# Optimization experiments

Hardware: AMD Instinct MI355X
Metric: run time of the kernel (lower is better)

Reference implementation:

```python
import jax, jax.numpy as jnp
import numpy as np

N_NODES = 100000
N_EDGES = 3200000
D_IN = 128
D_OUT = 128

def setup_inputs() -> dict:
    key = jax.random.key(0)
    k1, k2, k3, k4, k5 = jax.random.split(key, 5)
    nodes = jnp.arange(N_NODES, dtype=jnp.int64 if jax.config.jax_enable_x64 else jnp.int32)
    features = jax.random.normal(k1, (N_NODES, D_IN), dtype=jnp.float32)
    edge_index = jax.random.randint(k2, (2, N_EDGES), 0, N_NODES)
    # torch nn.Linear(2*D_IN, D_OUT) params, stored as [in, out]
    bound = 1.0 / np.sqrt(2 * D_IN)
    W = jax.random.uniform(k3, (2 * D_IN, D_OUT), minval=-bound, maxval=bound, dtype=jnp.float32)
    b = jax.random.uniform(k4, (D_OUT,), minval=-bound, maxval=bound, dtype=jnp.float32)
    return {"nodes": nodes, "features": features, "edge_index": edge_index, "W": W, "b": b}

def reference(nodes, features, edge_index, W, b):
    # Mean aggregation over full neighbor lists. gcn=False: edges are treated
    # as undirected (neighbors appended for both src and dst), and output is
    # relu(Linear(concat([self_feats, neigh_feats]))).
    N, d = features.shape
    src, dst = edge_index[0], edge_index[1]
    neigh_sum = (jnp.zeros((N, d), features.dtype)
                 .at[src].add(features[dst])
                 .at[dst].add(features[src]))
    cnt = (jnp.zeros((N,), features.dtype)
           .at[src].add(1.0)
           .at[dst].add(1.0))
    neigh_mean = neigh_sum / jnp.maximum(cnt, 1.0)[:, None]
    combined = jnp.concatenate([features[nodes], neigh_mean[nodes]], axis=1)  # [B, 2d]
    return jax.nn.relu(combined @ W + b)
```

## Files before the change

### kernel.cpp

```cpp
#include <hip/hip_runtime.h>
#include <hip/hip_bf16.h>
#include <cmath>

#define D 128
#define MAXNB 1024
#define TEDGE 4096
#define BSH 8
#define BNODES 256
#define CURPAD 16

typedef __attribute__((ext_vector_type(8))) short bf16x8;
typedef __attribute__((ext_vector_type(4))) float f32x4;
typedef __attribute__((ext_vector_type(2))) float f32x2;

__device__ __forceinline__ unsigned short f2bf(float f) {
    union { __hip_bfloat16 h; unsigned short u; } c;
    c.h = __float2bfloat16(f);
    return c.u;
}

__device__ __forceinline__ void accum8(float* a, uint4 u) {
    a[0] += __uint_as_float(u.x << 16);
    a[1] += __uint_as_float(u.x & 0xffff0000u);
    a[2] += __uint_as_float(u.y << 16);
    a[3] += __uint_as_float(u.y & 0xffff0000u);
    a[4] += __uint_as_float(u.z << 16);
    a[5] += __uint_as_float(u.z & 0xffff0000u);
    a[6] += __uint_as_float(u.w << 16);
    a[7] += __uint_as_float(u.w & 0xffff0000u);
}

__device__ __forceinline__ void accum8f8v(f32x2* a, uint2 u) {
    a[0] += __builtin_amdgcn_cvt_pk_f32_fp8((int)u.x, false);
    a[1] += __builtin_amdgcn_cvt_pk_f32_fp8((int)u.x, true);
    a[2] += __builtin_amdgcn_cvt_pk_f32_fp8((int)u.y, false);
    a[3] += __builtin_amdgcn_cvt_pk_f32_fp8((int)u.y, true);
}

__global__ __launch_bounds__(256) void partition_edges(
    const int* __restrict__ ei, int* __restrict__ cursor,
    int* __restrict__ arena, int pbcap, int E, int nb) {
    __shared__ int cnt[MAXNB];
    __shared__ int off[MAXNB + 1];
    __shared__ int gb[MAXNB];
    __shared__ int sb[256];
    __shared__ int stage[2 * TEDGE];
    const int t = threadIdx.x;
    const int e0 = blockIdx.x * TEDGE;
    const int eE = min(e0 + TEDGE, E);

#pragma unroll
    for (int k = 0; k < 4; ++k) cnt[t * 4 + k] = 0;
    __syncthreads();

    int s[16], d[16];
    bool v[16];
#pragma unroll
    for (int q = 0; q < 16; ++q) {
        int e = e0 + t + q * 256;
        v[q] = e < eE;
        if (v[q]) { s[q] = ei[e]; d[q] = ei[E + e]; }
    }

#pragma unroll
    for (int q = 0; q < 16; ++q) if (v[q]) {
        atomicAdd(&cnt[s[q] >> BSH], 1);
        atomicAdd(&cnt[d[q] >> BSH], 1);
    }
    __syncthreads();

    int c0 = cnt[t * 4], c1 = cnt[t * 4 + 1], c2 = cnt[t * 4 + 2], c3 = cnt[t * 4 + 3];
    sb[t] = c0 + c1 + c2 + c3;
    __syncthreads();
    for (int o = 1; o < 256; o <<= 1) {
        int x = (t >= o) ? sb[t - o] : 0;
        __syncthreads();
        sb[t] += x;
        __syncthreads();
    }
    int run = (t > 0) ? sb[t - 1] : 0;
    off[t * 4] = run; run += c0;
    off[t * 4 + 1] = run; run += c1;
    off[t * 4 + 2] = run; run += c2;
    off[t * 4 + 3] = run;
    if (t == 255) off[MAXNB] = sb[255];

    for (int j = t; j < nb; j += 256) {
        int c = cnt[j];
        gb[j] = c ? atomicAdd(&cursor[j * CURPAD], c) : 0;
    }
    __syncthreads();

#pragma unroll
    for (int k = 0; k < 4; ++k) cnt[t * 4 + k] = off[t * 4 + k];
    __syncthreads();

#pragma unroll
    for (int q = 0; q < 16; ++q) if (v[q]) {
        int ps = atomicAdd(&cnt[s[q] >> BSH], 1);
        stage[ps] = ((s[q] & (BNODES - 1)) << 17) | d[q];
        int pd = atomicAdd(&cnt[d[q] >> BSH], 1);
        stage[pd] = ((d[q] & (BNODES - 1)) << 17) | s[q];
    }
    __syncthreads();

    const int total = 2 * (eE - e0);
    for (int p = t; p < total; p += 256) {
        int vv = stage[p];
        int lo = 0, hi = MAXNB;
        while (hi - lo > 1) {
            int mid = (lo + hi) >> 1;
            if (off[mid] <= p) lo = mid; else hi = mid;
        }
        int idx = gb[lo] + (p - off[lo]);
        if (idx < pbcap) arena[(size_t)lo * pbcap + idx] = vv;
    }
}

__global__ __launch_bounds__(512) void bucket_scatter(
    const int* __restrict__ cursor, const int* __restrict__ arena, int pbcap,
    int* __restrict__ deg, int* __restrict__ colp, int cap, int N, int nb) {
    __shared__ int ldeg[BNODES];
    const int t = threadIdx.x;
    for (int b = blockIdx.x; b < nb; b += gridDim.x) {
        if (t < BNODES) ldeg[t] = 0;
        __syncthreads();
        int cnt = cursor[b * CURPAD];
        if (cnt > pbcap) cnt = pbcap;
        const int* s = arena + (size_t)b * pbcap;
        const size_t cb = ((size_t)b << BSH) * cap;
        int i = t;
        for (; i + 1536 < cnt; i += 2048) {
            int v0 = s[i], v1 = s[i + 512], v2 = s[i + 1024], v3 = s[i + 1536];
            int r0 = atomicAdd(&ldeg[v0 >> 17], 1);
            int r1 = atomicAdd(&ldeg[v1 >> 17], 1);
            int r2 = atomicAdd(&ldeg[v2 >> 17], 1);
            int r3 = atomicAdd(&ldeg[v3 >> 17], 1);
            if (r0 < cap) colp[cb + (size_t)(v0 >> 17) * cap + r0] = v0 & 0x1FFFF;
            if (r1 < cap) colp[cb + (size_t)(v1 >> 17) * cap + r1] = v1 & 0x1FFFF;
            if (r2 < cap) colp[cb + (size_t)(v2 >> 17) * cap + r2] = v2 & 0x1FFFF;
            if (r3 < cap) colp[cb + (size_t)(v3 >> 17) * cap + r3] = v3 & 0x1FFFF;
        }
        for (; i < cnt; i += 512) {
            int v = s[i];
            int r = atomicAdd(&ldeg[v >> 17], 1);
            if (r < cap) colp[cb + (size_t)(v >> 17) * cap + r] = v & 0x1FFFF;
        }
        __syncthreads();
        if (t < BNODES) {
            int node = (b << BSH) + t;
            if (node < N) deg[node] = ldeg[t];
        }
        __syncthreads();
    }
}

__global__ __launch_bounds__(256) void bucket_fill(
    const int* __restrict__ ei, int* __restrict__ deg,
    int* __restrict__ colp, int cap, int E) {
    int tid = blockIdx.x * blockDim.x + threadIdx.x;
    int stride = gridDim.x * blockDim.x;
    int e[8], s[8], d[8];
    bool v[8];
#pragma unroll
    for (int q = 0; q < 8; ++q) {
        e[q] = tid + q * stride;
        v[q] = e[q] < E;
    }
#pragma unroll
    for (int q = 0; q < 8; ++q) if (v[q]) { s[q] = ei[e[q]]; d[q] = ei[E + e[q]]; }
    int rs[8], rd[8];
#pragma unroll
    for (int q = 0; q < 8; ++q) if (v[q]) rs[q] = atomicAdd(&deg[s[q]], 1);
#pragma unroll
    for (int q = 0; q < 8; ++q) if (v[q]) rd[q] = atomicAdd(&deg[d[q]], 1);
#pragma unroll
    for (int q = 0; q < 8; ++q) if (v[q] && rs[q] < cap) colp[(size_t)s[q] * cap + rs[q]] = d[q];
#pragma unroll
    for (int q = 0; q < 8; ++q) if (v[q] && rd[q] < cap) colp[(size_t)d[q] * cap + rd[q]] = s[q];
}

__global__ __launch_bounds__(256) void prep_all(
    const float* __restrict__ feat, const float* __restrict__ W,
    int* __restrict__ cursor, uint2* __restrict__ f8,
    unsigned* __restrict__ wb, int n8) {
    const int tid = blockIdx.x * blockDim.x + threadIdx.x;
    const int stride = gridDim.x * blockDim.x;

    for (int i = tid; i < 1024 * CURPAD; i += stride) cursor[i] = 0;

    for (int id = tid; id < 4096; id += stride) {
        int j = id & 127, ks = id >> 7;
        unsigned hi[4], lo[4];
#pragma unroll
        for (int e = 0; e < 4; ++e) {
            float w0 = W[(size_t)(ks * 8 + 2 * e) * 128 + j];
            float w1 = W[(size_t)(ks * 8 + 2 * e + 1) * 128 + j];
            unsigned short h0 = f2bf(w0), h1 = f2bf(w1);
            float l0f = w0 - __uint_as_float((unsigned)h0 << 16);
            float l1f = w1 - __uint_as_float((unsigned)h1 << 16);
            hi[e] = (unsigned)h0 | ((unsigned)h1 << 16);
            lo[e] = (unsigned)f2bf(l0f) | ((unsigned)f2bf(l1f) << 16);
        }
        ((uint4*)wb)[ks * 128 + j] = make_uint4(hi[0], hi[1], hi[2], hi[3]);
        ((uint4*)wb)[4096 + ks * 128 + j] = make_uint4(lo[0], lo[1], lo[2], lo[3]);
    }

    const float4* f = (const float4*)feat;
    for (int i = tid; i < n8; i += stride) {
        float4 a = f[2 * i];
        float4 c = f[2 * i + 1];
        int w0 = __builtin_amdgcn_cvt_pk_fp8_f32(a.x, a.y, 0, false);
        w0 = __builtin_amdgcn_cvt_pk_fp8_f32(a.z, a.w, w0, true);
        int w1 = __builtin_amdgcn_cvt_pk_fp8_f32(c.x, c.y, 0, false);
        w1 = __builtin_amdgcn_cvt_pk_fp8_f32(c.z, c.w, w1, true);
        uint2 r;
        r.x = (unsigned)w0;
        r.y = (unsigned)w1;
        f8[i] = r;
    }
}

__global__ __launch_bounds__(256) void convert_fp8(
    const float4* __restrict__ f, uint2* __restrict__ o, int n8) {
    int i = blockIdx.x * blockDim.x + threadIdx.x;
    int stride = gridDim.x * blockDim.x;
    for (; i < n8; i += stride) {
        float4 a = f[2 * i];
        float4 c = f[2 * i + 1];
        int w0 = __builtin_amdgcn_cvt_pk_fp8_f32(a.x, a.y, 0, false);
        w0 = __builtin_amdgcn_cvt_pk_fp8_f32(a.z, a.w, w0, true);
        int w1 = __builtin_amdgcn_cvt_pk_fp8_f32(c.x, c.y, 0, false);
        w1 = __builtin_amdgcn_cvt_pk_fp8_f32(c.z, c.w, w1, true);
        uint2 r;
        r.x = (unsigned)w0;
        r.y = (unsigned)w1;
        o[i] = r;
    }
}

__global__ __launch_bounds__(256) void convert_bf16(
    const float4* __restrict__ f, uint2* __restrict__ o, int n4) {
    int i = blockIdx.x * blockDim.x + threadIdx.x;
    int stride = gridDim.x * blockDim.x;
    for (; i < n4; i += stride) {
        float4 v = f[i];
        uint2 r;
        r.x = (unsigned)f2bf(v.x) | ((unsigned)f2bf(v.y) << 16);
        r.y = (unsigned)f2bf(v.z) | ((unsigned)f2bf(v.w) << 16);
        o[i] = r;
    }
}

__global__ __launch_bounds__(256) void prepack_w(
    const float* __restrict__ W, unsigned* __restrict__ wb) {
    int id = blockIdx.x * 256 + threadIdx.x;
    if (id >= 4096) return;
    int j = id & 127, ks = id >> 7;
    unsigned hi[4], lo[4];
#pragma unroll
    for (int e = 0; e < 4; ++e) {
        float w0 = W[(size_t)(ks * 8 + 2 * e) * 128 + j];
        float w1 = W[(size_t)(ks * 8 + 2 * e + 1) * 128 + j];
        unsigned short h0 = f2bf(w0), h1 = f2bf(w1);
        float l0f = w0 - __uint_as_float((unsigned)h0 << 16);
        float l1f = w1 - __uint_as_float((unsigned)h1 << 16);
        hi[e] = (unsigned)h0 | ((unsigned)h1 << 16);
        lo[e] = (unsigned)f2bf(l0f) | ((unsigned)f2bf(l1f) << 16);
    }
    ((uint4*)wb)[ks * 128 + j] = make_uint4(hi[0], hi[1], hi[2], hi[3]);
    ((uint4*)wb)[4096 + ks * 128 + j] = make_uint4(lo[0], lo[1], lo[2], lo[3]);
}

__global__ __launch_bounds__(256) void gather_gemm_pad(
    const int* __restrict__ nodes, const float* __restrict__ feat,
    const uint2* __restrict__ fb2,
    const int* __restrict__ deg, const int* __restrict__ colp, int cap,
    const uint4* __restrict__ wb4, const float* __restrict__ b,
    float* __restrict__ out, int B) {
    __shared__ uint4 combQ[512];
    unsigned char* combB = (unsigned char*)combQ;
    const int t = threadIdx.x;
    const int lane = t & 63;
    const int w = t >> 6;
    const int g = lane >> 4;
    const int sub = lane & 15;
    const int base = blockIdx.x * 16;

    {
        int r = t >> 4, sb = t & 15;
        int row = base + r;
        uint4 u = make_uint4(0u, 0u, 0u, 0u);
        if (row < B) {
            const float* fp = feat + (size_t)nodes[row] * D + sb * 8;
            float4 a = *(const float4*)fp;
            float4 c = *(const float4*)(fp + 4);
            u.x = (unsigned)f2bf(a.x) | ((unsigned)f2bf(a.y) << 16);
            u.y = (unsigned)f2bf(a.z) | ((unsigned)f2bf(a.w) << 16);
            u.z = (unsigned)f2bf(c.x) | ((unsigned)f2bf(c.y) << 16);
            u.w = (unsigned)f2bf(c.z) | ((unsigned)f2bf(c.w) << 16);
        }
        int off = (r * 512 + sb * 16) ^ ((r & 7) << 4);
        *(uint4*)(combB + off) = u;
    }

    for (int rq = 0; rq < 4; ++rq) {
        const int rl = w + 4 * rq;
        const int row = base + rl;
        if (row < B) {
            const int node = __builtin_amdgcn_readfirstlane(nodes[row]);
            int degn = deg[node];
            if (degn > cap) degn = cap;
            const int p0 = node * cap;
            f32x2 accA[4] = {{0.f, 0.f}, {0.f, 0.f}, {0.f, 0.f}, {0.f, 0.f}};
            f32x2 accB[4] = {{0.f, 0.f}, {0.f, 0.f}, {0.f, 0.f}, {0.f, 0.f}};
            int i = 0;
            int nn0 = 0, nn1 = 0, nn2 = 0, nn3 = 0;
            if (degn >= 16) {
                nn0 = colp[p0 + g];
                nn1 = colp[p0 + 4 + g];
                nn2 = colp[p0 + 8 + g];
                nn3 = colp[p0 + 12 + g];
            }
            for (; i + 15 < degn; i += 16) {
                int n0 = nn0, n1 = nn1, n2 = nn2, n3 = nn3;
                if (i + 31 < degn) {
                    nn0 = colp[p0 + i + 16 + g];
                    nn1 = colp[p0 + i + 20 + g];
                    nn2 = colp[p0 + i + 24 + g];
                    nn3 = colp[p0 + i + 28 + g];
                }
                uint2 u0 = fb2[(size_t)n0 * 16 + sub];
                uint2 u1 = fb2[(size_t)n1 * 16 + sub];
                uint2 u2 = fb2[(size_t)n2 * 16 + sub];
                uint2 u3 = fb2[(size_t)n3 * 16 + sub];
                accum8f8v(accA, u0);
                accum8f8v(accB, u1);
                accum8f8v(accA, u2);
                accum8f8v(accB, u3);
            }
            for (; i + 7 < degn; i += 8) {
                int n0 = colp[p0 + i + g];
                int n1 = colp[p0 + i + 4 + g];
                uint2 u0 = fb2[(size_t)n0 * 16 + sub];
                uint2 u1 = fb2[(size_t)n1 * 16 + sub];
                accum8f8v(accA, u0);
                accum8f8v(accB, u1);
            }
            for (; i + 3 < degn; i += 4) {
                int n0 = colp[p0 + i + g];
                accum8f8v(accA, fb2[(size_t)n0 * 16 + sub]);
            }
            int rem = degn - i;
            if (g < rem) {
                int n0 = colp[p0 + i + g];
                accum8f8v(accB, fb2[(size_t)n0 * 16 + sub]);
            }
            const float inv = (degn > 0) ? 1.0f / (float)degn : 0.0f;
            float vals[8];
#pragma unroll
            for (int k = 0; k < 4; ++k) {
                f32x2 v2 = accA[k] + accB[k];
                float vx = v2.x, vy = v2.y;
                vx += __shfl_xor(vx, 16, 64);
                vx += __shfl_xor(vx, 32, 64);
                vy += __shfl_xor(vy, 16, 64);
                vy += __shfl_xor(vy, 32, 64);
                vals[2 * k] = vx * inv;
                vals[2 * k + 1] = vy * inv;
            }
            if (g == 0) {
                unsigned p0u = (unsigned)f2bf(vals[0]) | ((unsigned)f2bf(vals[1]) << 16);
                unsigned p1u = (unsigned)f2bf(vals[2]) | ((unsigned)f2bf(vals[3]) << 16);
                unsigned p2u = (unsigned)f2bf(vals[4]) | ((unsigned)f2bf(vals[5]) << 16);
                unsigned p3u = (unsigned)f2bf(vals[6]) | ((unsigned)f2bf(vals[7]) << 16);
                int off = (rl * 512 + 256 + sub * 16) ^ ((rl & 7) << 4);
                *(uint4*)(combB + off) = make_uint4(p0u, p1u, p2u, p3u);
            }
        } else if (g == 0) {
            int off = (rl * 512 + 256 + sub * 16) ^ ((rl & 7) << 4);
            *(uint4*)(combB + off) = make_uint4(0u, 0u, 0u, 0u);
        }
    }
    __syncthreads();

    const int jl = lane & 15;
    const int kg = lane >> 4;
    const int j0 = w * 32 + jl, j1 = j0 + 16;
    f32x4 acc0 = {0.f, 0.f, 0.f, 0.f};
    f32x4 acc1 = {0.f, 0.f, 0.f, 0.f};
#pragma unroll
    for (int s = 0; s < 8; ++s) {
        int aoff = (jl * 512 + s * 64 + kg * 16) ^ ((jl & 7) << 4);
        bf16x8 a = *(const bf16x8*)(combB + aoff);
        int bi = (s * 4 + kg) * 128;
        bf16x8 bh0 = *(const bf16x8*)&wb4[bi + j0];
        bf16x8 bh1 = *(const bf16x8*)&wb4[bi + j1];
        bf16x8 bl0 = *(const bf16x8*)&wb4[4096 + bi + j0];
        bf16x8 bl1 = *(const bf16x8*)&wb4[4096 + bi + j1];
        acc0 = __builtin_amdgcn_mfma_f32_16x16x32_bf16(a, bh0, acc0, 0, 0, 0);
        acc1 = __builtin_amdgcn_mfma_f32_16x16x32_bf16(a, bh1, acc1, 0, 0, 0);
        acc0 = __builtin_amdgcn_mfma_f32_16x16x32_bf16(a, bl0, acc0, 0, 0, 0);
        acc1 = __builtin_amdgcn_mfma_f32_16x16x32_bf16(a, bl1, acc1, 0, 0, 0);
    }
    const float b0 = b[j0], b1 = b[j1];
    const int r0 = kg * 4;
#pragma unroll
    for (int rg = 0; rg < 4; ++rg) {
        int row = base + r0 + rg;
        if (row < B) {
            out[(size_t)row * D + j0] = fmaxf(acc0[rg] + b0, 0.0f);
            out[(size_t)row * D + j1] = fmaxf(acc1[rg] + b1, 0.0f);
        }
    }
}


__global__ __launch_bounds__(256) void deg_rank(
    const int* __restrict__ ei, int* __restrict__ deg,
    unsigned* __restrict__ rank, int E) {
    int tid = blockIdx.x * blockDim.x + threadIdx.x;
    int stride = gridDim.x * blockDim.x;
    int e[8], s[8], d[8];
    bool v[8];
#pragma unroll
    for (int q = 0; q < 8; ++q) {
        e[q] = tid + q * stride;
        v[q] = e[q] < E;
    }
#pragma unroll
    for (int q = 0; q < 8; ++q) if (v[q]) { s[q] = ei[e[q]]; d[q] = ei[E + e[q]]; }
    int rs[8], rd[8];
#pragma unroll
    for (int q = 0; q < 8; ++q) if (v[q]) rs[q] = atomicAdd(&deg[s[q]], 1);
#pragma unroll
    for (int q = 0; q < 8; ++q) if (v[q]) rd[q] = atomicAdd(&deg[d[q]], 1);
#pragma unroll
    for (int q = 0; q < 8; ++q)
        if (v[q]) rank[e[q]] = (unsigned)rs[q] | ((unsigned)rd[q] << 16);
}

__global__ __launch_bounds__(256) void scan_block(
    const int* __restrict__ deg, int* __restrict__ rowptr,
    int* __restrict__ bsum, int N) {
    __shared__ int lds[256];
    const int t = threadIdx.x;
    const int base = blockIdx.x * 1024 + t * 4;
    int v[4];
#pragma unroll
    for (int k = 0; k < 4; ++k) v[k] = (base + k < N) ? deg[base + k] : 0;
    lds[t] = v[0] + v[1] + v[2] + v[3];
    __syncthreads();
    for (int off = 1; off < 256; off <<= 1) {
        int x = (t >= off) ? lds[t - off] : 0;
        __syncthreads();
        lds[t] += x;
        __syncthreads();
    }
    if (t == 255) bsum[blockIdx.x] = lds[255];
    int run = (t > 0) ? lds[t - 1] : 0;
#pragma unroll
    for (int k = 0; k < 4; ++k) {
        if (base + k < N) rowptr[base + k] = run;
        run += v[k];
    }
}

__global__ __launch_bounds__(1024) void scan_aux(int* __restrict__ bsum, int nb) {
    __shared__ int lds[1024];
    const int t = threadIdx.x;
    int v = (t < nb) ? bsum[t] : 0;
    lds[t] = v;
    __syncthreads();
    for (int off = 1; off < 1024; off <<= 1) {
        int x = (t >= off) ? lds[t - off] : 0;
        __syncthreads();
        lds[t] += x;
        __syncthreads();
    }
    if (t < nb) bsum[t] = lds[t] - v;
}

__global__ __launch_bounds__(256) void scan_finalize(
    int* __restrict__ rowptr, const int* __restrict__ bsum, int N, int twoE) {
    int i = blockIdx.x * blockDim.x + threadIdx.x;
    if (i == 0) rowptr[N] = twoE;
    if (i >= N) return;
    rowptr[i] += bsum[i >> 10];
}

__global__ __launch_bounds__(256) void csr_fill2(
    const int* __restrict__ ei, const int* __restrict__ rowptr,
    const unsigned* __restrict__ rank, int* __restrict__ col, int E) {
    int tid = blockIdx.x * blockDim.x + threadIdx.x;
    int stride = gridDim.x * blockDim.x;
    int e[8], s[8], d[8], ps[8], pd[8];
    unsigned r[8];
    bool v[8];
#pragma unroll
    for (int q = 0; q < 8; ++q) {
        e[q] = tid + q * stride;
        v[q] = e[q] < E;
    }
#pragma unroll
    for (int q = 0; q < 8; ++q) if (v[q]) { s[q] = ei[e[q]]; d[q] = ei[E + e[q]]; r[q] = rank[e[q]]; }
#pragma unroll
    for (int q = 0; q < 8; ++q) if (v[q]) { ps[q] = rowptr[s[q]]; pd[q] = rowptr[d[q]]; }
#pragma unroll
    for (int q = 0; q < 8; ++q) if (v[q]) {
        col[ps[q] + (int)(r[q] & 0xffffu)] = d[q];
        col[pd[q] + (int)(r[q] >> 16)] = s[q];
    }
}

__global__ __launch_bounds__(256) void gather_gemm(
    const int* __restrict__ nodes, const uint4* __restrict__ fb4,
    const int* __restrict__ rowptr, const int* __restrict__ col,
    const float* __restrict__ W, const float* __restrict__ b,
    float* __restrict__ out, int B) {
    __shared__ float comb[16][256];
    const int t = threadIdx.x;
    const int lane = t & 63;
    const int w = t >> 6;
    const int g = lane >> 4;
    const int sub = lane & 15;
    const int base = blockIdx.x * 16;
    {
        int r = t >> 4, sb = t & 15;
        int row = base + r;
        float a[8] = {0, 0, 0, 0, 0, 0, 0, 0};
        if (row < B) accum8(a, fb4[(size_t)nodes[row] * 16 + sb]);
        *(float4*)&comb[r][sb * 8] = make_float4(a[0], a[1], a[2], a[3]);
        *(float4*)&comb[r][sb * 8 + 4] = make_float4(a[4], a[5], a[6], a[7]);
    }
    for (int rq = 0; rq < 4; ++rq) {
        const int rl = w + 4 * rq;
        const int row = base + rl;
        if (row < B) {
            const int node = __builtin_amdgcn_readfirstlane(nodes[row]);
            const int p0 = rowptr[node], p1 = rowptr[node + 1];
            float accA[8] = {0, 0, 0, 0, 0, 0, 0, 0};
            float accB[8] = {0, 0, 0, 0, 0, 0, 0, 0};
            int i = p0;
            for (; i + 7 < p1; i += 8) {
                int na = col[i + g];
                int nb = col[i + 4 + g];
                uint4 ua = fb4[(size_t)na * 16 + sub];
                uint4 ub = fb4[(size_t)nb * 16 + sub];
                accum8(accA, ua);
                accum8(accB, ub);
            }
            for (; i + 3 < p1; i += 4) {
                int na = col[i + g];
                accum8(accA, fb4[(size_t)na * 16 + sub]);
            }
            int rem = p1 - i;
            if (g < rem) {
                int na = col[i + g];
                accum8(accB, fb4[(size_t)na * 16 + sub]);
            }
            const int degn = p1 - p0;
            const float inv = (degn > 0) ? 1.0f / (float)degn : 0.0f;
            float vals[8];
#pragma unroll
            for (int k = 0; k < 8; ++k) {
                float v = accA[k] + accB[k];
                v += __shfl_xor(v, 16, 64);
                v += __shfl_xor(v, 32, 64);
                vals[k] = v * inv;
            }
            if (g == 0) {
                *(float4*)&comb[rl][128 + sub * 8] =
                    make_float4(vals[0], vals[1], vals[2], vals[3]);
                *(float4*)&comb[rl][128 + sub * 8 + 4] =
                    make_float4(vals[4], vals[5], vals[6], vals[7]);
            }
        } else if (g == 0) {
            float4 z = make_float4(0.f, 0.f, 0.f, 0.f);
            *(float4*)&comb[rl][128 + sub * 8] = z;
            *(float4*)&comb[rl][128 + sub * 8 + 4] = z;
        }
    }
    __syncthreads();
    const int j = t & 127;
    const int rr = t >> 7;
    float acc[8];
    const float bj = b[j];
#pragma unroll
    for (int r = 0; r < 8; ++r) acc[r] = bj;
    for (int k4 = 0; k4 < 64; ++k4) {
        float w0 = W[(size_t)(4 * k4 + 0) * 128 + j];
        float w1 = W[(size_t)(4 * k4 + 1) * 128 + j];
        float w2 = W[(size_t)(4 * k4 + 2) * 128 + j];
        float w3 = W[(size_t)(4 * k4 + 3) * 128 + j];
#pragma unroll
        for (int r = 0; r < 8; ++r) {
            float4 c = *(const float4*)&comb[2 * r + rr][4 * k4];
            acc[r] = fmaf(c.x, w0, acc[r]);
            acc[r] = fmaf(c.y, w1, acc[r]);
            acc[r] = fmaf(c.z, w2, acc[r]);
            acc[r] = fmaf(c.w, w3, acc[r]);
        }
    }
#pragma unroll
    for (int r = 0; r < 8; ++r) {
        int row = base + 2 * r + rr;
        if (row < B) out[(size_t)row * D + j] = fmaxf(acc[r], 0.0f);
    }
}

__global__ __launch_bounds__(256) void edge_scatter(
    const int* __restrict__ ei, const float* __restrict__ feat,
    float* __restrict__ nsum, float* __restrict__ cnt, int E) {
    long long tid = (long long)blockIdx.x * blockDim.x + threadIdx.x;
    int e = (int)(tid >> 7);
    if (e >= E) return;
    int d = (int)(tid & 127);
    int src = ei[e];
    int dst = ei[E + e];
    atomicAdd(&nsum[(size_t)src * D + d], feat[(size_t)dst * D + d]);
    atomicAdd(&nsum[(size_t)dst * D + d], feat[(size_t)src * D + d]);
    if (d == 0) {
        atomicAdd(&cnt[src], 1.0f);
        atomicAdd(&cnt[dst], 1.0f);
    }
}

__global__ __launch_bounds__(256) void sage_out(
    const int* __restrict__ nodes, const float* __restrict__ feat,
    const float* nsum, const float* __restrict__ cnt,
    const float* __restrict__ W, const float* __restrict__ b,
    float* out, int B) {
    __shared__ float comb[16][256];
    const int t = threadIdx.x;
    const int j = t & 127;
    const int rr = t >> 7;
    const int base = blockIdx.x * 16;
    for (int r = 0; r < 16; ++r) {
        int row = base + r;
        float v = 0.0f;
        if (row < B) {
            int node = nodes[row];
            if (t < 128) v = feat[(size_t)node * D + t];
            else v = nsum[(size_t)node * D + (t - 128)] / fmaxf(cnt[node], 1.0f);
        }
        comb[r][t] = v;
    }
    __syncthreads();
    float acc[8];
    const float bj = b[j];
#pragma unroll
    for (int r = 0; r < 8; ++r) acc[r] = bj;
#pragma unroll 4
    for (int k = 0; k < 256; ++k) {
        float wj = W[(size_t)k * 128 + j];
#pragma unroll
        for (int r = 0; r < 8; ++r) acc[r] += comb[rr + 2 * r][k] * wj;
    }
#pragma unroll
    for (int r = 0; r < 8; ++r) {
        int row = base + rr + 2 * r;
        if (row < B) out[(size_t)row * D + j] = fmaxf(acc[r], 0.0f);
    }
}

extern "C" void kernel_launch(void* const* d_in, const int* in_sizes, int n_in,
                              void* d_out, int out_size, void* d_ws, size_t ws_size,
                              hipStream_t stream) {
    const int* nodes = (const int*)d_in[0];
    const float* feat = (const float*)d_in[1];
    const int* ei = (const int*)d_in[2];
    const float* W = (const float*)d_in[3];
    const float* b = (const float*)d_in[4];
    float* out = (float*)d_out;

    const int B = in_sizes[0];
    const int N = in_sizes[1] / D;
    const int E = in_sizes[2] / 2;
    const int twoE = 2 * E;
    const int nscan = (N + 1023) / 1024;
    const int n4 = N * (D / 4);
    const int n8 = N * (D / 8);
    const size_t ws_ints = ws_size / sizeof(int);

    const int nb = (N + BNODES - 1) >> BSH;
    double avgpb = nb > 0 ? (2.0 * (double)E) / (double)nb : 0.0;
    int pbcap = (int)(avgpb + 8.0 * sqrt(avgpb > 0.0 ? avgpb : 0.0) + 64.0);
    pbcap = (pbcap + 3) & ~3;
    const size_t u_arena = (size_t)nb * pbcap;
    const size_t u_fp8 = (size_t)N * 32;
    const size_t u0 = (u_arena > u_fp8) ? u_arena : u_fp8;
    const size_t o0_deg = (u0 + 3) & ~(size_t)3;
    const size_t o0_cur = (o0_deg + N + 3) & ~(size_t)3;
    const size_t o0_wb = o0_cur + 1024 * CURPAD;
    const size_t o0_colp = o0_wb + 32768;
    long long cap0_ll = (ws_ints > o0_colp) ? (long long)((ws_ints - o0_colp) / N) : 0;
    int cap0 = (cap0_ll > 192) ? 192 : (int)cap0_ll;

    const size_t o1_deg = (size_t)N * 32;
    const size_t o1_wb = (o1_deg + N + 3) & ~(size_t)3;
    const size_t o1_colp = o1_wb + 32768;
    long long cap_ll = (ws_ints > o1_colp) ? (long long)((ws_ints - o1_colp) / N) : 0;
    int cap = (cap_ll > 192) ? 192 : (int)cap_ll;

    const size_t o_deg = 0;
    const size_t o_rowptr = (o_deg + N + 3) & ~(size_t)3;
    const size_t o_bsum = (o_rowptr + N + 1 + 3) & ~(size_t)3;
    const size_t o_col = (o_bsum + 1024 + 3) & ~(size_t)3;
    const size_t o_rank = (o_col + twoE + 3) & ~(size_t)3;
    const size_t tail = ((size_t)E > (size_t)N * 64) ? (size_t)E : (size_t)N * 64;
    const size_t need2 = (o_rank + tail) * sizeof(int);

    if (cap0 >= 128 && N <= (1 << 17) && nb <= MAXNB && E > 0) {
        int* wsI = (int*)d_ws;
        int* arena = wsI;
        unsigned* f8 = (unsigned*)wsI;
        int* deg = wsI + o0_deg;
        int* cursor = wsI + o0_cur;
        unsigned* wbp = (unsigned*)(wsI + o0_wb);
        int* colp = wsI + o0_colp;

        prep_all<<<64, 256, 0, stream>>>(feat, W, cursor, (uint2*)f8, wbp, 0);

        int pblocks = (E + TEDGE - 1) / TEDGE;
        partition_edges<<<pblocks, 256, 0, stream>>>(ei, cursor, arena, pbcap, E, nb);

        bucket_scatter<<<nb, 512, 0, stream>>>(
            cursor, arena, pbcap, deg, colp, cap0, N, nb);

        convert_fp8<<<(n8 + 1023) / 1024, 256, 0, stream>>>(
            (const float4*)feat, (uint2*)f8, n8);

        gather_gemm_pad<<<(B + 15) / 16, 256, 0, stream>>>(
            nodes, feat, (const uint2*)f8, deg, colp, cap0,
            (const uint4*)wbp, b, out, B);
    } else if (cap >= 128) {
        int* wsI = (int*)d_ws;
        unsigned* f8 = (unsigned*)wsI;
        int* deg = wsI + o1_deg;
        unsigned* wbp = (unsigned*)(wsI + o1_wb);
        int* colp = wsI + o1_colp;

        hipMemsetAsync(deg, 0, (size_t)N * sizeof(int), stream);

        prepack_w<<<16, 256, 0, stream>>>(W, wbp);

        convert_fp8<<<(n8 + 1023) / 1024, 256, 0, stream>>>(
            (const float4*)feat, (uint2*)f8, n8);

        int eb8 = (E + 2047) / 2048;
        bucket_fill<<<eb8, 256, 0, stream>>>(ei, deg, colp, cap, E);

        gather_gemm_pad<<<(B + 15) / 16, 256, 0, stream>>>(
            nodes, feat, (const uint2*)f8, deg, colp, cap,
            (const uint4*)wbp, b, out, B);
    } else if (ws_size >= need2 && nscan <= 1024) {
        int* wsI = (int*)d_ws;
        int* deg = wsI + o_deg;
        int* rowptr = wsI + o_rowptr;
        int* bsum = wsI + o_bsum;
        int* col = wsI + o_col;
        unsigned* rank = (unsigned*)(wsI + o_rank);
        unsigned* fbu = (unsigned*)(wsI + o_rank);

        hipMemsetAsync(deg, 0, (size_t)N * sizeof(int), stream);

        int eb8 = (E + 2047) / 2048;
        deg_rank<<<eb8, 256, 0, stream>>>(ei, deg, rank, E);
        scan_block<<<nscan, 256, 0, stream>>>(deg, rowptr, bsum, N);
        scan_aux<<<1, 1024, 0, stream>>>(bsum, nscan);
        scan_finalize<<<(N + 255) / 256, 256, 0, stream>>>(rowptr, bsum, N, twoE);
        csr_fill2<<<eb8, 256, 0, stream>>>(ei, rowptr, rank, col, E);
        convert_bf16<<<(n4 + 1023) / 1024, 256, 0, stream>>>(
            (const float4*)feat, (uint2*)fbu, n4);
        gather_gemm<<<(B + 15) / 16, 256, 0, stream>>>(
            nodes, (const uint4*)fbu, rowptr, col, W, b, out, B);
    } else {
        float* nsum = out;
        float* cnt = (float*)d_ws;
        hipMemsetAsync(d_out, 0, (size_t)N * D * sizeof(float), stream);
        hipMemsetAsync(d_ws, 0, (size_t)N * sizeof(float), stream);
        long long tot = (long long)E * 128;
        int blocks = (int)((tot + 255) / 256);
        edge_scatter<<<blocks, 256, 0, stream>>>(ei, feat, nsum, cnt, E);
        sage_out<<<(B + 15) / 16, 256, 0, stream>>>(nodes, feat, nsum, cnt, W, b, out, B);
    }
}
```

Measured before the change: 381.1 us.

## Fuse fp8 conversion into bucket_scatter and stage neighbor lists in LDS

Gives the fp8 feature buffer its own workspace region so it no longer aliases the edge arena. That lets extra blocks of the bucket_scatter launch run the fp32-to-fp8 conversion alongside the scatter, which removes the separate convert_fp8 launch. The gather kernel now preloads per-row degrees and column indices into LDS with coalesced loads before the gather loop, in place of the per-wave register prefetch from global memory. This costs more workspace, which gates the new path, and more LDS per block, which may reduce occupancy.

```diff
diff --git a/kernel.cpp b/kernel.cpp
--- a/kernel.cpp
+++ b/kernel.cpp
@@ -8,6 +8,7 @@
 #define BSH 8
 #define BNODES 256
 #define CURPAD 16
+#define LCS 200
 
 typedef __attribute__((ext_vector_type(8))) short bf16x8;
 typedef __attribute__((ext_vector_type(4))) float f32x4;
@@ -119,39 +120,56 @@
 
 __global__ __launch_bounds__(512) void bucket_scatter(
     const int* __restrict__ cursor, const int* __restrict__ arena, int pbcap,
-    int* __restrict__ deg, int* __restrict__ colp, int cap, int N, int nb) {
+    int* __restrict__ deg, int* __restrict__ colp, int cap, int N, int nb,
+    const float4* __restrict__ feat4, uint2* __restrict__ f8, int n8, int nconv) {
     __shared__ int ldeg[BNODES];
     const int t = threadIdx.x;
-    for (int b = blockIdx.x; b < nb; b += gridDim.x) {
-        if (t < BNODES) ldeg[t] = 0;
-        __syncthreads();
-        int cnt = cursor[b * CURPAD];
-        if (cnt > pbcap) cnt = pbcap;
-        const int* s = arena + (size_t)b * pbcap;
-        const size_t cb = ((size_t)b << BSH) * cap;
-        int i = t;
-        for (; i + 1536 < cnt; i += 2048) {
-            int v0 = s[i], v1 = s[i + 512], v2 = s[i + 1024], v3 = s[i + 1536];
-            int r0 = atomicAdd(&ldeg[v0 >> 17], 1);
-            int r1 = atomicAdd(&ldeg[v1 >> 17], 1);
-            int r2 = atomicAdd(&ldeg[v2 >> 17], 1);
-            int r3 = atomicAdd(&ldeg[v3 >> 17], 1);
-            if (r0 < cap) colp[cb + (size_t)(v0 >> 17) * cap + r0] = v0 & 0x1FFFF;
-            if (r1 < cap) colp[cb + (size_t)(v1 >> 17) * cap + r1] = v1 & 0x1FFFF;
-            if (r2 < cap) colp[cb + (size_t)(v2 >> 17) * cap + r2] = v2 & 0x1FFFF;
-            if (r3 < cap) colp[cb + (size_t)(v3 >> 17) * cap + r3] = v3 & 0x1FFFF;
-        }
-        for (; i < cnt; i += 512) {
-            int v = s[i];
-            int r = atomicAdd(&ldeg[v >> 17], 1);
-            if (r < cap) colp[cb + (size_t)(v >> 17) * cap + r] = v & 0x1FFFF;
-        }
-        __syncthreads();
-        if (t < BNODES) {
-            int node = (b << BSH) + t;
-            if (node < N) deg[node] = ldeg[t];
-        }
-        __syncthreads();
+    const int bx = (int)blockIdx.x;
+    if (bx >= nb) {
+        int i = (bx - nb) * (int)blockDim.x + t;
+        const int stride = nconv * (int)blockDim.x;
+        for (; i < n8; i += stride) {
+            float4 a = feat4[2 * i];
+            float4 c = feat4[2 * i + 1];
+            int w0 = __builtin_amdgcn_cvt_pk_fp8_f32(a.x, a.y, 0, false);
+            w0 = __builtin_amdgcn_cvt_pk_fp8_f32(a.z, a.w, w0, true);
+            int w1 = __builtin_amdgcn_cvt_pk_fp8_f32(c.x, c.y, 0, false);
+            w1 = __builtin_amdgcn_cvt_pk_fp8_f32(c.z, c.w, w1, true);
+            uint2 r;
+            r.x = (unsigned)w0;
+            r.y = (unsigned)w1;
+            f8[i] = r;
+        }
+        return;
+    }
+    const int b = bx;
+    if (t < BNODES) ldeg[t] = 0;
+    __syncthreads();
+    int cnt = cursor[b * CURPAD];
+    if (cnt > pbcap) cnt = pbcap;
+    const int* s = arena + (size_t)b * pbcap;
+    const size_t cb = ((size_t)b << BSH) * cap;
+    int i = t;
+    for (; i + 1536 < cnt; i += 2048) {
+        int v0 = s[i], v1 = s[i + 512], v2 = s[i + 1024], v3 = s[i + 1536];
+        int r0 = atomicAdd(&ldeg[v0 >> 17], 1);
+        int r1 = atomicAdd(&ldeg[v1 >> 17], 1);
+        int r2 = atomicAdd(&ldeg[v2 >> 17], 1);
+        int r3 = atomicAdd(&ldeg[v3 >> 17], 1);
+        if (r0 < cap) colp[cb + (size_t)(v0 >> 17) * cap + r0] = v0 & 0x1FFFF;
+        if (r1 < cap) colp[cb + (size_t)(v1 >> 17) * cap + r1] = v1 & 0x1FFFF;
+        if (r2 < cap) colp[cb + (size_t)(v2 >> 17) * cap + r2] = v2 & 0x1FFFF;
+        if (r3 < cap) colp[cb + (size_t)(v3 >> 17) * cap + r3] = v3 & 0x1FFFF;
+    }
+    for (; i < cnt; i += 512) {
+        int v = s[i];
+        int r = atomicAdd(&ldeg[v >> 17], 1);
+        if (r < cap) colp[cb + (size_t)(v >> 17) * cap + r] = v & 0x1FFFF;
+    }
+    __syncthreads();
+    if (t < BNODES) {
+        int node = (b << BSH) + t;
+        if (node < N) deg[node] = ldeg[t];
     }
 }
 
@@ -279,6 +297,8 @@
     const uint4* __restrict__ wb4, const float* __restrict__ b,
     float* __restrict__ out, int B) {
     __shared__ uint4 combQ[512];
+    __shared__ int sdeg[16];
+    __shared__ int lcol[16 * LCS];
     unsigned char* combB = (unsigned char*)combQ;
     const int t = threadIdx.x;
     const int lane = t & 63;
@@ -287,6 +307,15 @@
     const int sub = lane & 15;
     const int base = blockIdx.x * 16;
 
+    if (t < 16) {
+        int row = base + t;
+        int dgv = 0;
+        if (row < B) {
+            dgv = deg[nodes[row]];
+            if (dgv > cap) dgv = cap;
+        }
+        sdeg[t] = dgv;
+    }
     {
         int r = t >> 4, sb = t & 15;
         int row = base + r;
@@ -303,83 +332,77 @@
         int off = (r * 512 + sb * 16) ^ ((r & 7) << 4);
         *(uint4*)(combB + off) = u;
     }
+    __syncthreads();
+
+    {
+        int r = t >> 4, l = t & 15;
+        int row = base + r;
+        int dgv = sdeg[r];
+        if (row < B && dgv > 0) {
+            int p0 = nodes[row] * cap;
+            for (int i = l; i < dgv; i += 16) lcol[r * LCS + i] = colp[p0 + i];
+        }
+    }
+    __syncthreads();
 
     for (int rq = 0; rq < 4; ++rq) {
         const int rl = w + 4 * rq;
-        const int row = base + rl;
-        if (row < B) {
-            const int node = __builtin_amdgcn_readfirstlane(nodes[row]);
-            int degn = deg[node];
-            if (degn > cap) degn = cap;
-            const int p0 = node * cap;
-            f32x2 accA[4] = {{0.f, 0.f}, {0.f, 0.f}, {0.f, 0.f}, {0.f, 0.f}};
-            f32x2 accB[4] = {{0.f, 0.f}, {0.f, 0.f}, {0.f, 0.f}, {0.f, 0.f}};
-            int i = 0;
-            int nn0 = 0, nn1 = 0, nn2 = 0, nn3 = 0;
-            if (degn >= 16) {
-                nn0 = colp[p0 + g];
-                nn1 = colp[p0 + 4 + g];
-                nn2 = colp[p0 + 8 + g];
-                nn3 = colp[p0 + 12 + g];
-            }
-            for (; i + 15 < degn; i += 16) {
-                int n0 = nn0, n1 = nn1, n2 = nn2, n3 = nn3;
-                if (i + 31 < degn) {
-                    nn0 = colp[p0 + i + 16 + g];
-                    nn1 = colp[p0 + i + 20 + g];
-                    nn2 = colp[p0 + i + 24 + g];
-                    nn3 = colp[p0 + i + 28 + g];
-                }
-                uint2 u0 = fb2[(size_t)n0 * 16 + sub];
-                uint2 u1 = fb2[(size_t)n1 * 16 + sub];
-                uint2 u2 = fb2[(size_t)n2 * 16 + sub];
-                uint2 u3 = fb2[(size_t)n3 * 16 + sub];
-                accum8f8v(accA, u0);
-                accum8f8v(accB, u1);
-                accum8f8v(accA, u2);
-                accum8f8v(accB, u3);
-            }
-            for (; i + 7 < degn; i += 8) {
-                int n0 = colp[p0 + i + g];
-                int n1 = colp[p0 + i + 4 + g];
-                uint2 u0 = fb2[(size_t)n0 * 16 + sub];
-                uint2 u1 = fb2[(size_t)n1 * 16 + sub];
-                accum8f8v(accA, u0);
-                accum8f8v(accB, u1);
-            }
-            for (; i + 3 < degn; i += 4) {
-                int n0 = colp[p0 + i + g];
-                accum8f8v(accA, fb2[(size_t)n0 * 16 + sub]);
-            }
-            int rem = degn - i;
-            if (g < rem) {
-                int n0 = colp[p0 + i + g];
-                accum8f8v(accB, fb2[(size_t)n0 * 16 + sub]);
-            }
-            const float inv = (degn > 0) ? 1.0f / (float)degn : 0.0f;
-            float vals[8];
-#pragma unroll
-            for (int k = 0; k < 4; ++k) {
-                f32x2 v2 = accA[k] + accB[k];
-                float vx = v2.x, vy = v2.y;
-                vx += __shfl_xor(vx, 16, 64);
-                vx += __shfl_xor(vx, 32, 64);
-                vy += __shfl_xor(vy, 16, 64);
-                vy += __shfl_xor(vy, 32, 64);
-                vals[2 * k] = vx * inv;
-                vals[2 * k + 1] = vy * inv;
-            }
-            if (g == 0) {
-                unsigned p0u = (unsigned)f2bf(vals[0]) | ((unsigned)f2bf(vals[1]) << 16);
-                unsigned p1u = (unsigned)f2bf(vals[2]) | ((unsigned)f2bf(vals[3]) << 16);
-                unsigned p2u = (unsigned)f2bf(vals[4]) | ((unsigned)f2bf(vals[5]) << 16);
-                unsigned p3u = (unsigned)f2bf(vals[6]) | ((unsigned)f2bf(vals[7]) << 16);
-                int off = (rl * 512 + 256 + sub * 16) ^ ((rl & 7) << 4);
-                *(uint4*)(combB + off) = make_uint4(p0u, p1u, p2u, p3u);
-            }
-        } else if (g == 0) {
+        const int degn = sdeg[rl];
+        const int* lc = &lcol[rl * LCS];
+        f32x2 accA[4] = {{0.f, 0.f}, {0.f, 0.f}, {0.f, 0.f}, {0.f, 0.f}};
+        f32x2 accB[4] = {{0.f, 0.f}, {0.f, 0.f}, {0.f, 0.f}, {0.f, 0.f}};
+        int i = 0;
+        for (; i + 15 < degn; i += 16) {
+            int n0 = lc[i + g];
+            int n1 = lc[i + 4 + g];
+            int n2 = lc[i + 8 + g];
+            int n3 = lc[i + 12 + g];
+            uint2 u0 = fb2[(size_t)n0 * 16 + sub];
+            uint2 u1 = fb2[(size_t)n1 * 16 + sub];
+            uint2 u2 = fb2[(size_t)n2 * 16 + sub];
+            uint2 u3 = fb2[(size_t)n3 * 16 + sub];
+            accum8f8v(accA, u0);
+            accum8f8v(accB, u1);
+            accum8f8v(accA, u2);
+            accum8f8v(accB, u3);
+        }
+        for (; i + 7 < degn; i += 8) {
+            int n0 = lc[i + g];
+            int n1 = lc[i + 4 + g];
+            uint2 u0 = fb2[(size_t)n0 * 16 + sub];
+            uint2 u1 = fb2[(size_t)n1 * 16 + sub];
+            accum8f8v(accA, u0);
+            accum8f8v(accB, u1);
+        }
+        for (; i + 3 < degn; i += 4) {
+            int n0 = lc[i + g];
+            accum8f8v(accA, fb2[(size_t)n0 * 16 + sub]);
+        }
+        int rem = degn - i;
+        if (g < rem) {
+            int n0 = lc[i + g];
+            accum8f8v(accB, fb2[(size_t)n0 * 16 + sub]);
+        }
+        const float inv = (degn > 0) ? 1.0f / (float)degn : 0.0f;
+        float vals[8];
+#pragma unroll
+        for (int k = 0; k < 4; ++k) {
+            f32x2 v2 = accA[k] + accB[k];
+            float vx = v2.x, vy = v2.y;
+            vx += __shfl_xor(vx, 16, 64);
+            vx += __shfl_xor(vx, 32, 64);
+            vy += __shfl_xor(vy, 16, 64);
+            vy += __shfl_xor(vy, 32, 64);
+            vals[2 * k] = vx * inv;
+            vals[2 * k + 1] = vy * inv;
+        }
+        if (g == 0) {
+            unsigned p0u = (unsigned)f2bf(vals[0]) | ((unsigned)f2bf(vals[1]) << 16);
+            unsigned p1u = (unsigned)f2bf(vals[2]) | ((unsigned)f2bf(vals[3]) << 16);
+            unsigned p2u = (unsigned)f2bf(vals[4]) | ((unsigned)f2bf(vals[5]) << 16);
+            unsigned p3u = (unsigned)f2bf(vals[6]) | ((unsigned)f2bf(vals[7]) << 16);
             int off = (rl * 512 + 256 + sub * 16) ^ ((rl & 7) << 4);
-            *(uint4*)(combB + off) = make_uint4(0u, 0u, 0u, 0u);
+            *(uint4*)(combB + off) = make_uint4(p0u, p1u, p2u, p3u);
         }
     }
     __syncthreads();
@@ -689,6 +712,15 @@
     pbcap = (pbcap + 3) & ~3;
     const size_t u_arena = (size_t)nb * pbcap;
     const size_t u_fp8 = (size_t)N * 32;
+
+    const size_t sF_f8 = (u_arena + 3) & ~(size_t)3;
+    const size_t sF_deg = (sF_f8 + u_fp8 + 3) & ~(size_t)3;
+    const size_t sF_cur = (sF_deg + N + 3) & ~(size_t)3;
+    const size_t sF_wb = sF_cur + 1024 * CURPAD;
+    const size_t sF_colp = sF_wb + 32768;
+    long long capF_ll = (ws_ints > sF_colp) ? (long long)((ws_ints - sF_colp) / N) : 0;
+    int capF = (capF_ll > 192) ? 192 : (int)capF_ll;
+
     const size_t u0 = (u_arena > u_fp8) ? u_arena : u_fp8;
     const size_t o0_deg = (u0 + 3) & ~(size_t)3;
     const size_t o0_cur = (o0_deg + N + 3) & ~(size_t)3;
@@ -711,7 +743,31 @@
     const size_t tail = ((size_t)E > (size_t)N * 64) ? (size_t)E : (size_t)N * 64;
     const size_t need2 = (o_rank + tail) * sizeof(int);
 
-    if (cap0 >= 128 && N <= (1 << 17) && nb <= MAXNB && E > 0) {
+    const bool t0ok = (N <= (1 << 17)) && (nb <= MAXNB) && (E > 0);
+
+    if (capF >= 128 && t0ok) {
+        int* wsI = (int*)d_ws;
+        int* arena = wsI;
+        unsigned* f8 = (unsigned*)(wsI + sF_f8);
+        int* deg = wsI + sF_deg;
+        int* cursor = wsI + sF_cur;
+        unsigned* wbp = (unsigned*)(wsI + sF_wb);
+        int* colp = wsI + sF_colp;
+
+        prep_all<<<64, 256, 0, stream>>>(feat, W, cursor, (uint2*)f8, wbp, 0);
+
+        int pblocks = (E + TEDGE - 1) / TEDGE;
+        partition_edges<<<pblocks, 256, 0, stream>>>(ei, cursor, arena, pbcap, E, nb);
+
+        const int CVTB = 256;
+        bucket_scatter<<<nb + CVTB, 512, 0, stream>>>(
+            cursor, arena, pbcap, deg, colp, capF, N, nb,
+            (const float4*)feat, (uint2*)f8, n8, CVTB);
+
+        gather_gemm_pad<<<(B + 15) / 16, 256, 0, stream>>>(
+            nodes, feat, (const uint2*)f8, deg, colp, capF,
+            (const uint4*)wbp, b, out, B);
+    } else if (cap0 >= 128 && t0ok) {
         int* wsI = (int*)d_ws;
         int* arena = wsI;
         unsigned* f8 = (unsigned*)wsI;
@@ -726,7 +782,8 @@
         partition_edges<<<pblocks, 256, 0, stream>>>(ei, cursor, arena, pbcap, E, nb);
 
         bucket_scatter<<<nb, 512, 0, stream>>>(
-            cursor, arena, pbcap, deg, colp, cap0, N, nb);
+            cursor, arena, pbcap, deg, colp, cap0, N, nb,
+            (const float4*)nullptr, (uint2*)nullptr, 0, 0);
 
         convert_fp8<<<(n8 + 1023) / 1024, 256, 0, stream>>>(
             (const float4*)feat, (uint2*)f8, n8);
```

Measured after the change: 438.3 us. +15.0%, slower.
